# Kernel optimization log

Hardware: AMD Instinct MI355X
Metric: run time of the kernel (lower is better)

The kernel has to match this reference:

```python
import jax, jax.numpy as jnp
import numpy as np

# SOM hyperparameters (match init_kwargs)
M, N = 64, 64
NODES = M * N
FEATS = 256
BATCH = 1024
LR = 0.5
RADIUS_FACTOR = 1.1
TOTAL_ITER = 100000
SIGMA = max(M, N) * RADIUS_FACTOR


def setup_inputs() -> dict:
    key = jax.random.key(0)
    k1, k2 = jax.random.split(key)
    x = jax.random.uniform(k1, (BATCH, FEATS), dtype=jnp.float32)
    map_w = jax.random.uniform(k2, (NODES, FEATS), dtype=jnp.float32)
    return {"x": x, "map_w": map_w, "iteration": 0}


def _grid_locs():
    ii, jj = jnp.meshgrid(jnp.arange(M), jnp.arange(N), indexing='ij')
    return jnp.stack([ii.ravel(), jj.ravel()], axis=1)  # (NODES, 2) int32


def reference(x, map_w, iteration):
    B = x.shape[0]
    # ---- feedforward: squared distances (B, NODES) via GEMM expansion,
    # avoiding the (B, NODES, FEATS) broadcast the TF code materializes.
    x2 = jnp.sum(x * x, axis=1, keepdims=True)          # (B, 1)
    w2 = jnp.sum(map_w * map_w, axis=1)                  # (NODES,)
    sqd = x2 + w2[None, :] - 2.0 * (x @ map_w.T)         # (B, NODES)
    bmu_indices = jnp.argmin(sqd, axis=1)                # (B,)

    # ---- backprop: neighborhood-weighted codebook update
    locs = _grid_locs()                                  # (NODES, 2)
    bmu_locs = locs[bmu_indices]                         # (B, 2)
    # grid distance^2 between every node and each sample's BMU: (B, NODES)
    d2 = jnp.sum((locs[None, :, :] - bmu_locs[:, None, :]) ** 2, axis=2).astype(jnp.float32)

    lambda_g = TOTAL_ITER / SIGMA
    decay = jnp.exp(jnp.float32(-float(iteration) / lambda_g))
    radius = SIGMA * decay + 1e-6
    lr = LR * decay

    impact = jnp.exp(-d2 / (2.0 * radius * radius))
    in_radius = (jnp.sqrt(d2) <= radius).astype(jnp.float32)
    lr_op = impact * in_radius * lr                      # (B, NODES)

    # weight_update[n,d] = sum_b lr_op[b,n] * (x[b,d] - map_w[n,d])
    # computed without the (B, NODES, FEATS) intermediate:
    upd = (jnp.einsum('bn,bd->nd', lr_op, x) - lr_op.sum(axis=0)[:, None] * map_w) / B
    new_map = map_w + upd
    return new_map, bmu_indices
```

## Files before the change

kernel.cpp:

```cpp
#include <hip/hip_runtime.h>
#include <math.h>

#define NODES 4096
#define FEATS 256
#define BATCH 1024
#define LR_C 0.5f
#define SIGMA_C 70.4f

typedef _Float16 f16x8 __attribute__((ext_vector_type(8)));
typedef float floatx4 __attribute__((ext_vector_type(4)));

__device__ __forceinline__ void get_params(int it, float& lr, float& r2, float& i2r2) {
    float decay = __expf(-(float)it * (SIGMA_C / 100000.0f));
    float radius = SIGMA_C * decay + 1e-6f;
    lr = LR_C * decay;
    r2 = radius * radius;
    i2r2 = 1.0f / (2.0f * r2);
}

__device__ __forceinline__ unsigned fkey(float f) {
    unsigned u = __float_as_uint(f);
    return (u & 0x80000000u) ? ~u : (u | 0x80000000u);
}
__device__ __forceinline__ unsigned long long shfl_xor_u64(unsigned long long v, int mask) {
    unsigned lo = (unsigned)v, hi = (unsigned)(v >> 32);
    lo = __shfl_xor(lo, mask, 64);
    hi = __shfl_xor(hi, mask, 64);
    return ((unsigned long long)hi << 32) | lo;
}

__global__ __launch_bounds__(256) void k_prep(const float* __restrict__ Wm, const float* __restrict__ X,
                                              _Float16* __restrict__ Whi, _Float16* __restrict__ Wlo,
                                              float* __restrict__ w2,
                                              _Float16* __restrict__ Xhi, _Float16* __restrict__ Xlo,
                                              _Float16* __restrict__ XT,
                                              unsigned long long* __restrict__ gmin) {
    __shared__ _Float16 T[64][72];
    const int t = threadIdx.x;
    const int blk = blockIdx.x;
    const int wave = t >> 6, lane = t & 63;
#pragma unroll
    for (int rr = 0; rr < 2; ++rr) {
        int row = blk * 8 + wave * 2 + rr;
        float4 v = *(const float4*)&Wm[(size_t)row * FEATS + lane * 4];
        union { _Float16 h[4]; float2 f2; } uh, ul;
        uh.h[0] = (_Float16)v.x; uh.h[1] = (_Float16)v.y;
        uh.h[2] = (_Float16)v.z; uh.h[3] = (_Float16)v.w;
        ul.h[0] = (_Float16)(v.x - (float)uh.h[0]);
        ul.h[1] = (_Float16)(v.y - (float)uh.h[1]);
        ul.h[2] = (_Float16)(v.z - (float)uh.h[2]);
        ul.h[3] = (_Float16)(v.w - (float)uh.h[3]);
        *(float2*)&Whi[(size_t)row * FEATS + lane * 4] = uh.f2;
        *(float2*)&Wlo[(size_t)row * FEATS + lane * 4] = ul.f2;
        float s = v.x * v.x + v.y * v.y + v.z * v.z + v.w * v.w;
#pragma unroll
        for (int off = 32; off > 0; off >>= 1) s += __shfl_down(s, off, 64);
        if (lane == 0) w2[row] = s;
    }
    if (blk < 4) gmin[blk * 256 + t] = 0xFFFFFFFFFFFFFFFFULL;
    if (blk < 64) {
        const int b0 = (blk & 15) * 64, d0 = (blk >> 4) * 64;
        {
            const int bl = t >> 2, dq = (t & 3) * 16;
            union { _Float16 h[16]; float4 q[2]; } uh, ul;
#pragma unroll
            for (int c = 0; c < 4; ++c) {
                float4 v = *(const float4*)&X[(size_t)(b0 + bl) * FEATS + d0 + dq + c * 4];
                uh.h[c * 4 + 0] = (_Float16)v.x; uh.h[c * 4 + 1] = (_Float16)v.y;
                uh.h[c * 4 + 2] = (_Float16)v.z; uh.h[c * 4 + 3] = (_Float16)v.w;
                ul.h[c * 4 + 0] = (_Float16)(v.x - (float)uh.h[c * 4 + 0]);
                ul.h[c * 4 + 1] = (_Float16)(v.y - (float)uh.h[c * 4 + 1]);
                ul.h[c * 4 + 2] = (_Float16)(v.z - (float)uh.h[c * 4 + 2]);
                ul.h[c * 4 + 3] = (_Float16)(v.w - (float)uh.h[c * 4 + 3]);
            }
            *(float4*)&Xhi[(size_t)(b0 + bl) * FEATS + d0 + dq] = uh.q[0];
            *(float4*)&Xhi[(size_t)(b0 + bl) * FEATS + d0 + dq + 8] = uh.q[1];
            *(float4*)&Xlo[(size_t)(b0 + bl) * FEATS + d0 + dq] = ul.q[0];
            *(float4*)&Xlo[(size_t)(b0 + bl) * FEATS + d0 + dq + 8] = ul.q[1];
#pragma unroll
            for (int c = 0; c < 16; ++c) T[bl][dq + c] = uh.h[c];
        }
        __syncthreads();
        {
            const int dl = t >> 2, bq = (t & 3) * 16;
            union { _Float16 h[16]; float4 q[2]; } u;
#pragma unroll
            for (int c = 0; c < 16; ++c) u.h[c] = T[bq + c][dl];
            *(float4*)&XT[(size_t)(d0 + dl) * BATCH + b0 + bq] = u.q[0];
            *(float4*)&XT[(size_t)(d0 + dl) * BATCH + b0 + bq + 8] = u.q[1];
        }
    }
}

__global__ __launch_bounds__(256) void k_gemm1min(const _Float16* __restrict__ Xhi, const _Float16* __restrict__ Xlo,
                                                  const _Float16* __restrict__ Whi, const _Float16* __restrict__ Wlo,
                                                  const float* __restrict__ w2,
                                                  unsigned long long* __restrict__ gmin) {
    __shared__ _Float16 Ah[64][40];
    __shared__ _Float16 Al[64][40];
    __shared__ _Float16 Bh[64][40];
    __shared__ _Float16 Bl[64][40];
    __shared__ unsigned long long rowmin[64][2];
    const int n0 = blockIdx.x * 64;
    const int b0 = blockIdx.y * 64;
    const int t = threadIdx.x;
    const int wave = t >> 6, lane = t & 63;
    const int wm = wave & 1, wn = wave >> 1;
    const int lm = lane & 15, quad = lane >> 4;
    const int srow = t >> 2, skoff = (t & 3) * 8;
    floatx4 acc[2][2] = {};
    for (int k0 = 0; k0 < FEATS; k0 += 32) {
        *(float4*)&Ah[srow][skoff] = *(const float4*)&Xhi[(size_t)(b0 + srow) * FEATS + k0 + skoff];
        *(float4*)&Al[srow][skoff] = *(const float4*)&Xlo[(size_t)(b0 + srow) * FEATS + k0 + skoff];
        *(float4*)&Bh[srow][skoff] = *(const float4*)&Whi[(size_t)(n0 + srow) * FEATS + k0 + skoff];
        *(float4*)&Bl[srow][skoff] = *(const float4*)&Wlo[(size_t)(n0 + srow) * FEATS + k0 + skoff];
        __syncthreads();
        f16x8 ah[2], al[2], bh[2], bl[2];
        ah[0] = *(f16x8*)&Ah[wm * 32 + lm][quad * 8];
        ah[1] = *(f16x8*)&Ah[wm * 32 + 16 + lm][quad * 8];
        al[0] = *(f16x8*)&Al[wm * 32 + lm][quad * 8];
        al[1] = *(f16x8*)&Al[wm * 32 + 16 + lm][quad * 8];
        bh[0] = *(f16x8*)&Bh[wn * 32 + lm][quad * 8];
        bh[1] = *(f16x8*)&Bh[wn * 32 + 16 + lm][quad * 8];
        bl[0] = *(f16x8*)&Bl[wn * 32 + lm][quad * 8];
        bl[1] = *(f16x8*)&Bl[wn * 32 + 16 + lm][quad * 8];
#pragma unroll
        for (int i = 0; i < 2; ++i)
#pragma unroll
            for (int j = 0; j < 2; ++j) {
                acc[i][j] = __builtin_amdgcn_mfma_f32_16x16x32_f16(ah[i], bh[j], acc[i][j], 0, 0, 0);
                acc[i][j] = __builtin_amdgcn_mfma_f32_16x16x32_f16(ah[i], bl[j], acc[i][j], 0, 0, 0);
                acc[i][j] = __builtin_amdgcn_mfma_f32_16x16x32_f16(al[i], bh[j], acc[i][j], 0, 0, 0);
            }
        __syncthreads();
    }
    const int col0 = n0 + wn * 32 + lm, col1 = col0 + 16;
    const float w20 = w2[col0], w21 = w2[col1];
#pragma unroll
    for (int i = 0; i < 2; ++i) {
#pragma unroll
        for (int r = 0; r < 4; ++r) {
            float va = w20 - 2.0f * acc[i][0][r];
            float vb = w21 - 2.0f * acc[i][1][r];
            unsigned long long ka = ((unsigned long long)fkey(va) << 32) | (unsigned)col0;
            unsigned long long kb = ((unsigned long long)fkey(vb) << 32) | (unsigned)col1;
            unsigned long long m = ka < kb ? ka : kb;
#pragma unroll
            for (int mk = 1; mk < 16; mk <<= 1) {
                unsigned long long o = shfl_xor_u64(m, mk);
                if (o < m) m = o;
            }
            if (lm == 0) rowmin[wm * 32 + i * 16 + quad * 4 + r][wn] = m;
        }
    }
    __syncthreads();
    if (t < 64) {
        unsigned long long v = rowmin[t][0];
        if (rowmin[t][1] < v) v = rowmin[t][1];
        atomicMin(&gmin[b0 + t], v);
    }
}

__global__ __launch_bounds__(256) void k_lropB(const unsigned long long* __restrict__ gmin,
                                               const int* __restrict__ itp,
                                               _Float16* __restrict__ lrT, float* __restrict__ Svec,
                                               float* __restrict__ out1) {
    __shared__ int bmu_s[1024];
    __shared__ float texp[64];
    __shared__ float red4[4];
    const int t = threadIdx.x;
    const int blk = blockIdx.x;
#pragma unroll
    for (int j = 0; j < 4; ++j)
        bmu_s[t + j * 256] = (int)(gmin[t + j * 256] & 0xFFFFFFFFULL);
    float lr, r2, i2r2;
    get_params(itp[0], lr, r2, i2r2);
    if (t < 64) texp[t] = __expf(-(float)(t * t) * i2r2);
    __syncthreads();
    if (blk < 4) out1[blk * 256 + t] = (float)bmu_s[blk * 256 + t];
    const int n = blk * 2 + (t >> 7);
    const int b0 = (t & 127) * 8;
    const int ni = n >> 6, nj = n & 63;
    float s = 0.0f;
    union { _Float16 h[8]; float4 q; } u;
#pragma unroll
    for (int c = 0; c < 8; ++c) {
        int m = bmu_s[b0 + c];
        int di = ni - (m >> 6); di = di < 0 ? -di : di;
        int dj = nj - (m & 63); dj = dj < 0 ? -dj : dj;
        int d2 = di * di + dj * dj;
        float val = ((float)d2 <= r2) ? lr * texp[di] * texp[dj] : 0.0f;
        u.h[c] = (_Float16)val;
        s += val;
    }
    *(float4*)&lrT[(size_t)n * BATCH + b0] = u.q;
    const int lane = t & 63, wave = t >> 6;
#pragma unroll
    for (int off = 32; off > 0; off >>= 1) s += __shfl_down(s, off, 64);
    if (lane == 0) red4[wave] = s;
    __syncthreads();
    if (t < 2) Svec[blk * 2 + t] = red4[2 * t] + red4[2 * t + 1];
}

__global__ __launch_bounds__(256) void k_gemm2c(const _Float16* __restrict__ lrT, const _Float16* __restrict__ XT,
                                                const float* __restrict__ Svec, const float* __restrict__ Wm,
                                                float* __restrict__ out0) {
    __shared__ _Float16 As[32][136];
    __shared__ _Float16 Bs[64][136];
    __shared__ float Svl[32];
    const int d0 = blockIdx.x * 64;
    const int n0 = blockIdx.y * 32;
    const int t = threadIdx.x;
    const int wave = t >> 6, lane = t & 63;
    const int wm = wave & 1, wn = wave >> 1;
    const int lm = lane & 15, quad = lane >> 4;
    if (t < 32) Svl[t] = Svec[n0 + t];
    const int arow = t >> 3, acoff = (t & 7) * 16;
    const int brow = t >> 2, bcoff = (t & 3) * 32;
    floatx4 acc0 = {}, acc1 = {};
    for (int k0 = 0; k0 < BATCH; k0 += 128) {
        *(float4*)&As[arow][acoff] = *(const float4*)&lrT[(size_t)(n0 + arow) * BATCH + k0 + acoff];
        *(float4*)&As[arow][acoff + 8] = *(const float4*)&lrT[(size_t)(n0 + arow) * BATCH + k0 + acoff + 8];
#pragma unroll
        for (int c = 0; c < 4; ++c)
            *(float4*)&Bs[brow][bcoff + c * 8] =
                *(const float4*)&XT[(size_t)(d0 + brow) * BATCH + k0 + bcoff + c * 8];
        __syncthreads();
#pragma unroll
        for (int ks = 0; ks < 128; ks += 32) {
            f16x8 a = *(f16x8*)&As[wm * 16 + lm][ks + quad * 8];
            f16x8 b0 = *(f16x8*)&Bs[wn * 32 + lm][ks + quad * 8];
            f16x8 b1 = *(f16x8*)&Bs[wn * 32 + 16 + lm][ks + quad * 8];
            acc0 = __builtin_amdgcn_mfma_f32_16x16x32_f16(a, b0, acc0, 0, 0, 0);
            acc1 = __builtin_amdgcn_mfma_f32_16x16x32_f16(a, b1, acc1, 0, 0, 0);
        }
        __syncthreads();
    }
    const float invB = 1.0f / (float)BATCH;
#pragma unroll
    for (int r = 0; r < 4; ++r) {
        int rowN = n0 + wm * 16 + quad * 4 + r;
        float cc = 1.0f - Svl[rowN - n0] * invB;
        int col0 = d0 + wn * 32 + lm;
        int col1 = col0 + 16;
        out0[(size_t)rowN * FEATS + col0] = Wm[(size_t)rowN * FEATS + col0] * cc + acc0[r] * invB;
        out0[(size_t)rowN * FEATS + col1] = Wm[(size_t)rowN * FEATS + col1] * cc + acc1[r] * invB;
    }
}

extern "C" void kernel_launch(void* const* d_in, const int* in_sizes, int n_in,
                              void* d_out, int out_size, void* d_ws, size_t ws_size,
                              hipStream_t stream) {
    const float* X = (const float*)d_in[0];
    const float* Wm = (const float*)d_in[1];
    const int* itp = (const int*)d_in[2];
    float* out0 = (float*)d_out;
    float* out1 = out0 + (size_t)NODES * FEATS;

    char* ws = (char*)d_ws;
    float* w2       = (float*)(ws + 0);
    _Float16* Xhi   = (_Float16*)(ws + 16384);
    _Float16* Xlo   = (_Float16*)(ws + 540672);
    _Float16* XT    = (_Float16*)(ws + 1064960);
    _Float16* Whi   = (_Float16*)(ws + 1589248);
    _Float16* Wlo   = (_Float16*)(ws + 3686400);
    unsigned long long* gmin = (unsigned long long*)(ws + 5783552);
    float* Svec     = (float*)(ws + 5791744);
    _Float16* lrT   = (_Float16*)(ws + 5808128);

    k_prep<<<512, 256, 0, stream>>>(Wm, X, Whi, Wlo, w2, Xhi, Xlo, XT, gmin);
    k_gemm1min<<<dim3(64, 16), 256, 0, stream>>>(Xhi, Xlo, Whi, Wlo, w2, gmin);
    k_lropB<<<2048, 256, 0, stream>>>(gmin, itp, lrT, Svec, out1);
    k_gemm2c<<<dim3(4, 128), 256, 0, stream>>>(lrT, XT, Svec, Wm, out0);
}
```

Measured before the change: 95.84 us.

## Fuse fp16 split conversion into GEMM1 and merge XT transpose into lr kernel

Removes the separate prep kernel. GEMM1 now reads fp32 X and W directly, splits them into hi/lo fp16 in registers, and computes the W row norms on the fly. Its block tile grows to 128 rows with a per-wave atomicMin in place of the shared-memory row reduction. The X transpose to fp16 is appended as extra blocks of the lr-op kernel, and gmin is initialised with a memset. This saves one launch and the round trip of the fp16 copies through memory, at the cost of redoing the conversion in every GEMM block and issuing more atomics.

```diff
diff --git a/kernel.cpp b/kernel.cpp
--- a/kernel.cpp
+++ b/kernel.cpp
@@ -29,56 +29,158 @@
     return ((unsigned long long)hi << 32) | lo;
 }
 
-__global__ __launch_bounds__(256) void k_prep(const float* __restrict__ Wm, const float* __restrict__ X,
-                                              _Float16* __restrict__ Whi, _Float16* __restrict__ Wlo,
-                                              float* __restrict__ w2,
-                                              _Float16* __restrict__ Xhi, _Float16* __restrict__ Xlo,
-                                              _Float16* __restrict__ XT,
-                                              unsigned long long* __restrict__ gmin) {
-    __shared__ _Float16 T[64][72];
+__global__ __launch_bounds__(256) void k_gemm1min(const float* __restrict__ X, const float* __restrict__ Wm,
+                                                  unsigned long long* __restrict__ gmin) {
+    __shared__ _Float16 Ah[128][40];
+    __shared__ _Float16 Al[128][40];
+    __shared__ _Float16 Bh[64][40];
+    __shared__ _Float16 Bl[64][40];
+    __shared__ float w2s[64];
+    const int n0 = blockIdx.x * 64;
+    const int b0 = blockIdx.y * 128;
     const int t = threadIdx.x;
+    const int wave = t >> 6, lane = t & 63;
+    const int lm = lane & 15, quad = lane >> 4;
+    const int arow = t >> 1, ako = (t & 1) * 16;
+    const int brow = t >> 2, bko = (t & 3) * 8;
+    float w2p = 0.0f;
+    floatx4 acc[2][4] = {};
+    for (int k0 = 0; k0 < FEATS; k0 += 32) {
+        {
+            union { _Float16 h[16]; float4 q[2]; } uh, ul;
+#pragma unroll
+            for (int c = 0; c < 4; ++c) {
+                float4 v = *(const float4*)&X[(size_t)(b0 + arow) * FEATS + k0 + ako + c * 4];
+                _Float16 h0 = (_Float16)v.x, h1 = (_Float16)v.y, h2 = (_Float16)v.z, h3 = (_Float16)v.w;
+                uh.h[c * 4 + 0] = h0; uh.h[c * 4 + 1] = h1; uh.h[c * 4 + 2] = h2; uh.h[c * 4 + 3] = h3;
+                ul.h[c * 4 + 0] = (_Float16)(v.x - (float)h0);
+                ul.h[c * 4 + 1] = (_Float16)(v.y - (float)h1);
+                ul.h[c * 4 + 2] = (_Float16)(v.z - (float)h2);
+                ul.h[c * 4 + 3] = (_Float16)(v.w - (float)h3);
+            }
+            *(float4*)&Ah[arow][ako] = uh.q[0];
+            *(float4*)&Ah[arow][ako + 8] = uh.q[1];
+            *(float4*)&Al[arow][ako] = ul.q[0];
+            *(float4*)&Al[arow][ako + 8] = ul.q[1];
+        }
+        {
+            union { _Float16 h[8]; float4 q; } uh, ul;
+#pragma unroll
+            for (int c = 0; c < 2; ++c) {
+                float4 v = *(const float4*)&Wm[(size_t)(n0 + brow) * FEATS + k0 + bko + c * 4];
+                w2p += v.x * v.x + v.y * v.y + v.z * v.z + v.w * v.w;
+                _Float16 h0 = (_Float16)v.x, h1 = (_Float16)v.y, h2 = (_Float16)v.z, h3 = (_Float16)v.w;
+                uh.h[c * 4 + 0] = h0; uh.h[c * 4 + 1] = h1; uh.h[c * 4 + 2] = h2; uh.h[c * 4 + 3] = h3;
+                ul.h[c * 4 + 0] = (_Float16)(v.x - (float)h0);
+                ul.h[c * 4 + 1] = (_Float16)(v.y - (float)h1);
+                ul.h[c * 4 + 2] = (_Float16)(v.z - (float)h2);
+                ul.h[c * 4 + 3] = (_Float16)(v.w - (float)h3);
+            }
+            *(float4*)&Bh[brow][bko] = uh.q;
+            *(float4*)&Bl[brow][bko] = ul.q;
+        }
+        __syncthreads();
+        f16x8 ah[2], al[2], bh[4], bl[4];
+#pragma unroll
+        for (int i = 0; i < 2; ++i) {
+            ah[i] = *(f16x8*)&Ah[wave * 32 + i * 16 + lm][quad * 8];
+            al[i] = *(f16x8*)&Al[wave * 32 + i * 16 + lm][quad * 8];
+        }
+#pragma unroll
+        for (int j = 0; j < 4; ++j) {
+            bh[j] = *(f16x8*)&Bh[j * 16 + lm][quad * 8];
+            bl[j] = *(f16x8*)&Bl[j * 16 + lm][quad * 8];
+        }
+#pragma unroll
+        for (int i = 0; i < 2; ++i)
+#pragma unroll
+            for (int j = 0; j < 4; ++j) {
+                acc[i][j] = __builtin_amdgcn_mfma_f32_16x16x32_f16(ah[i], bh[j], acc[i][j], 0, 0, 0);
+                acc[i][j] = __builtin_amdgcn_mfma_f32_16x16x32_f16(ah[i], bl[j], acc[i][j], 0, 0, 0);
+                acc[i][j] = __builtin_amdgcn_mfma_f32_16x16x32_f16(al[i], bh[j], acc[i][j], 0, 0, 0);
+            }
+        __syncthreads();
+    }
+    w2p += __shfl_xor(w2p, 1, 64);
+    w2p += __shfl_xor(w2p, 2, 64);
+    if ((t & 3) == 0) w2s[brow] = w2p;
+    __syncthreads();
+#pragma unroll
+    for (int i = 0; i < 2; ++i)
+#pragma unroll
+        for (int r = 0; r < 4; ++r) {
+            const int row = b0 + wave * 32 + i * 16 + quad * 4 + r;
+            unsigned long long m = 0xFFFFFFFFFFFFFFFFULL;
+#pragma unroll
+            for (int j = 0; j < 4; ++j) {
+                float v = w2s[j * 16 + lm] - 2.0f * acc[i][j][r];
+                unsigned long long k = ((unsigned long long)fkey(v) << 32) | (unsigned)(n0 + j * 16 + lm);
+                if (k < m) m = k;
+            }
+#pragma unroll
+            for (int mk = 1; mk < 16; mk <<= 1) {
+                unsigned long long o = shfl_xor_u64(m, mk);
+                if (o < m) m = o;
+            }
+            if (lm == 0) atomicMin(&gmin[row], m);
+        }
+}
+
+__global__ __launch_bounds__(256) void k_lropX(const unsigned long long* __restrict__ gmin,
+                                               const int* __restrict__ itp, const float* __restrict__ X,
+                                               _Float16* __restrict__ lrT, float* __restrict__ Svec,
+                                               _Float16* __restrict__ XT, float* __restrict__ out1) {
     const int blk = blockIdx.x;
-    const int wave = t >> 6, lane = t & 63;
-#pragma unroll
-    for (int rr = 0; rr < 2; ++rr) {
-        int row = blk * 8 + wave * 2 + rr;
-        float4 v = *(const float4*)&Wm[(size_t)row * FEATS + lane * 4];
-        union { _Float16 h[4]; float2 f2; } uh, ul;
-        uh.h[0] = (_Float16)v.x; uh.h[1] = (_Float16)v.y;
-        uh.h[2] = (_Float16)v.z; uh.h[3] = (_Float16)v.w;
-        ul.h[0] = (_Float16)(v.x - (float)uh.h[0]);
-        ul.h[1] = (_Float16)(v.y - (float)uh.h[1]);
-        ul.h[2] = (_Float16)(v.z - (float)uh.h[2]);
-        ul.h[3] = (_Float16)(v.w - (float)uh.h[3]);
-        *(float2*)&Whi[(size_t)row * FEATS + lane * 4] = uh.f2;
-        *(float2*)&Wlo[(size_t)row * FEATS + lane * 4] = ul.f2;
-        float s = v.x * v.x + v.y * v.y + v.z * v.z + v.w * v.w;
+    const int t = threadIdx.x;
+    if (blk < 2048) {
+        __shared__ int bmu_s[1024];
+        __shared__ float texp[64];
+        __shared__ float red4[4];
+#pragma unroll
+        for (int j = 0; j < 4; ++j)
+            bmu_s[t + j * 256] = (int)(gmin[t + j * 256] & 0xFFFFFFFFULL);
+        float lr, r2, i2r2;
+        get_params(itp[0], lr, r2, i2r2);
+        if (t < 64) texp[t] = __expf(-(float)(t * t) * i2r2);
+        __syncthreads();
+        if (blk < 4) out1[blk * 256 + t] = (float)bmu_s[blk * 256 + t];
+        const int n = blk * 2 + (t >> 7);
+        const int b0 = (t & 127) * 8;
+        const int ni = n >> 6, nj = n & 63;
+        float s = 0.0f;
+        union { _Float16 h[8]; float4 q; } u;
+#pragma unroll
+        for (int c = 0; c < 8; ++c) {
+            int m = bmu_s[b0 + c];
+            int di = ni - (m >> 6); di = di < 0 ? -di : di;
+            int dj = nj - (m & 63); dj = dj < 0 ? -dj : dj;
+            int d2 = di * di + dj * dj;
+            float val = ((float)d2 <= r2) ? lr * texp[di] * texp[dj] : 0.0f;
+            u.h[c] = (_Float16)val;
+            s += val;
+        }
+        *(float4*)&lrT[(size_t)n * BATCH + b0] = u.q;
+        const int lane = t & 63, wave = t >> 6;
 #pragma unroll
         for (int off = 32; off > 0; off >>= 1) s += __shfl_down(s, off, 64);
-        if (lane == 0) w2[row] = s;
-    }
-    if (blk < 4) gmin[blk * 256 + t] = 0xFFFFFFFFFFFFFFFFULL;
-    if (blk < 64) {
-        const int b0 = (blk & 15) * 64, d0 = (blk >> 4) * 64;
+        if (lane == 0) red4[wave] = s;
+        __syncthreads();
+        if (t < 2) Svec[blk * 2 + t] = red4[2 * t] + red4[2 * t + 1];
+    } else {
+        __shared__ _Float16 T[64][72];
+        const int blk2 = blk - 2048;
+        const int b0 = (blk2 & 15) * 64, d0 = (blk2 >> 4) * 64;
         {
             const int bl = t >> 2, dq = (t & 3) * 16;
-            union { _Float16 h[16]; float4 q[2]; } uh, ul;
+            union { _Float16 h[16]; } u;
 #pragma unroll
             for (int c = 0; c < 4; ++c) {
                 float4 v = *(const float4*)&X[(size_t)(b0 + bl) * FEATS + d0 + dq + c * 4];
-                uh.h[c * 4 + 0] = (_Float16)v.x; uh.h[c * 4 + 1] = (_Float16)v.y;
-                uh.h[c * 4 + 2] = (_Float16)v.z; uh.h[c * 4 + 3] = (_Float16)v.w;
-                ul.h[c * 4 + 0] = (_Float16)(v.x - (float)uh.h[c * 4 + 0]);
-                ul.h[c * 4 + 1] = (_Float16)(v.y - (float)uh.h[c * 4 + 1]);
-                ul.h[c * 4 + 2] = (_Float16)(v.z - (float)uh.h[c * 4 + 2]);
-                ul.h[c * 4 + 3] = (_Float16)(v.w - (float)uh.h[c * 4 + 3]);
-            }
-            *(float4*)&Xhi[(size_t)(b0 + bl) * FEATS + d0 + dq] = uh.q[0];
-            *(float4*)&Xhi[(size_t)(b0 + bl) * FEATS + d0 + dq + 8] = uh.q[1];
-            *(float4*)&Xlo[(size_t)(b0 + bl) * FEATS + d0 + dq] = ul.q[0];
-            *(float4*)&Xlo[(size_t)(b0 + bl) * FEATS + d0 + dq + 8] = ul.q[1];
-#pragma unroll
-            for (int c = 0; c < 16; ++c) T[bl][dq + c] = uh.h[c];
+                u.h[c * 4 + 0] = (_Float16)v.x; u.h[c * 4 + 1] = (_Float16)v.y;
+                u.h[c * 4 + 2] = (_Float16)v.z; u.h[c * 4 + 3] = (_Float16)v.w;
+            }
+#pragma unroll
+            for (int c = 0; c < 16; ++c) T[bl][dq + c] = u.h[c];
         }
         __syncthreads();
         {
@@ -90,116 +192,6 @@
             *(float4*)&XT[(size_t)(d0 + dl) * BATCH + b0 + bq + 8] = u.q[1];
         }
     }
-}
-
-__global__ __launch_bounds__(256) void k_gemm1min(const _Float16* __restrict__ Xhi, const _Float16* __restrict__ Xlo,
-                                                  const _Float16* __restrict__ Whi, const _Float16* __restrict__ Wlo,
-                                                  const float* __restrict__ w2,
-                                                  unsigned long long* __restrict__ gmin) {
-    __shared__ _Float16 Ah[64][40];
-    __shared__ _Float16 Al[64][40];
-    __shared__ _Float16 Bh[64][40];
-    __shared__ _Float16 Bl[64][40];
-    __shared__ unsigned long long rowmin[64][2];
-    const int n0 = blockIdx.x * 64;
-    const int b0 = blockIdx.y * 64;
-    const int t = threadIdx.x;
-    const int wave = t >> 6, lane = t & 63;
-    const int wm = wave & 1, wn = wave >> 1;
-    const int lm = lane & 15, quad = lane >> 4;
-    const int srow = t >> 2, skoff = (t & 3) * 8;
-    floatx4 acc[2][2] = {};
-    for (int k0 = 0; k0 < FEATS; k0 += 32) {
-        *(float4*)&Ah[srow][skoff] = *(const float4*)&Xhi[(size_t)(b0 + srow) * FEATS + k0 + skoff];
-        *(float4*)&Al[srow][skoff] = *(const float4*)&Xlo[(size_t)(b0 + srow) * FEATS + k0 + skoff];
-        *(float4*)&Bh[srow][skoff] = *(const float4*)&Whi[(size_t)(n0 + srow) * FEATS + k0 + skoff];
-        *(float4*)&Bl[srow][skoff] = *(const float4*)&Wlo[(size_t)(n0 + srow) * FEATS + k0 + skoff];
-        __syncthreads();
-        f16x8 ah[2], al[2], bh[2], bl[2];
-        ah[0] = *(f16x8*)&Ah[wm * 32 + lm][quad * 8];
-        ah[1] = *(f16x8*)&Ah[wm * 32 + 16 + lm][quad * 8];
-        al[0] = *(f16x8*)&Al[wm * 32 + lm][quad * 8];
-        al[1] = *(f16x8*)&Al[wm * 32 + 16 + lm][quad * 8];
-        bh[0] = *(f16x8*)&Bh[wn * 32 + lm][quad * 8];
-        bh[1] = *(f16x8*)&Bh[wn * 32 + 16 + lm][quad * 8];
-        bl[0] = *(f16x8*)&Bl[wn * 32 + lm][quad * 8];
-        bl[1] = *(f16x8*)&Bl[wn * 32 + 16 + lm][quad * 8];
-#pragma unroll
-        for (int i = 0; i < 2; ++i)
-#pragma unroll
-            for (int j = 0; j < 2; ++j) {
-                acc[i][j] = __builtin_amdgcn_mfma_f32_16x16x32_f16(ah[i], bh[j], acc[i][j], 0, 0, 0);
-                acc[i][j] = __builtin_amdgcn_mfma_f32_16x16x32_f16(ah[i], bl[j], acc[i][j], 0, 0, 0);
-                acc[i][j] = __builtin_amdgcn_mfma_f32_16x16x32_f16(al[i], bh[j], acc[i][j], 0, 0, 0);
-            }
-        __syncthreads();
-    }
-    const int col0 = n0 + wn * 32 + lm, col1 = col0 + 16;
-    const float w20 = w2[col0], w21 = w2[col1];
-#pragma unroll
-    for (int i = 0; i < 2; ++i) {
-#pragma unroll
-        for (int r = 0; r < 4; ++r) {
-            float va = w20 - 2.0f * acc[i][0][r];
-            float vb = w21 - 2.0f * acc[i][1][r];
-            unsigned long long ka = ((unsigned long long)fkey(va) << 32) | (unsigned)col0;
-            unsigned long long kb = ((unsigned long long)fkey(vb) << 32) | (unsigned)col1;
-            unsigned long long m = ka < kb ? ka : kb;
-#pragma unroll
-            for (int mk = 1; mk < 16; mk <<= 1) {
-                unsigned long long o = shfl_xor_u64(m, mk);
-                if (o < m) m = o;
-            }
-            if (lm == 0) rowmin[wm * 32 + i * 16 + quad * 4 + r][wn] = m;
-        }
-    }
-    __syncthreads();
-    if (t < 64) {
-        unsigned long long v = rowmin[t][0];
-        if (rowmin[t][1] < v) v = rowmin[t][1];
-        atomicMin(&gmin[b0 + t], v);
-    }
-}
-
-__global__ __launch_bounds__(256) void k_lropB(const unsigned long long* __restrict__ gmin,
-                                               const int* __restrict__ itp,
-                                               _Float16* __restrict__ lrT, float* __restrict__ Svec,
-                                               float* __restrict__ out1) {
-    __shared__ int bmu_s[1024];
-    __shared__ float texp[64];
-    __shared__ float red4[4];
-    const int t = threadIdx.x;
-    const int blk = blockIdx.x;
-#pragma unroll
-    for (int j = 0; j < 4; ++j)
-        bmu_s[t + j * 256] = (int)(gmin[t + j * 256] & 0xFFFFFFFFULL);
-    float lr, r2, i2r2;
-    get_params(itp[0], lr, r2, i2r2);
-    if (t < 64) texp[t] = __expf(-(float)(t * t) * i2r2);
-    __syncthreads();
-    if (blk < 4) out1[blk * 256 + t] = (float)bmu_s[blk * 256 + t];
-    const int n = blk * 2 + (t >> 7);
-    const int b0 = (t & 127) * 8;
-    const int ni = n >> 6, nj = n & 63;
-    float s = 0.0f;
-    union { _Float16 h[8]; float4 q; } u;
-#pragma unroll
-    for (int c = 0; c < 8; ++c) {
-        int m = bmu_s[b0 + c];
-        int di = ni - (m >> 6); di = di < 0 ? -di : di;
-        int dj = nj - (m & 63); dj = dj < 0 ? -dj : dj;
-        int d2 = di * di + dj * dj;
-        float val = ((float)d2 <= r2) ? lr * texp[di] * texp[dj] : 0.0f;
-        u.h[c] = (_Float16)val;
-        s += val;
-    }
-    *(float4*)&lrT[(size_t)n * BATCH + b0] = u.q;
-    const int lane = t & 63, wave = t >> 6;
-#pragma unroll
-    for (int off = 32; off > 0; off >>= 1) s += __shfl_down(s, off, 64);
-    if (lane == 0) red4[wave] = s;
-    __syncthreads();
-    if (t < 2) Svec[blk * 2 + t] = red4[2 * t] + red4[2 * t + 1];
 }
 
 __global__ __launch_bounds__(256) void k_gemm2c(const _Float16* __restrict__ lrT, const _Float16* __restrict__ XT,
@@ -258,18 +250,13 @@
     float* out1 = out0 + (size_t)NODES * FEATS;
 
     char* ws = (char*)d_ws;
-    float* w2       = (float*)(ws + 0);
-    _Float16* Xhi   = (_Float16*)(ws + 16384);
-    _Float16* Xlo   = (_Float16*)(ws + 540672);
-    _Float16* XT    = (_Float16*)(ws + 1064960);
-    _Float16* Whi   = (_Float16*)(ws + 1589248);
-    _Float16* Wlo   = (_Float16*)(ws + 3686400);
-    unsigned long long* gmin = (unsigned long long*)(ws + 5783552);
-    float* Svec     = (float*)(ws + 5791744);
-    _Float16* lrT   = (_Float16*)(ws + 5808128);
-
-    k_prep<<<512, 256, 0, stream>>>(Wm, X, Whi, Wlo, w2, Xhi, Xlo, XT, gmin);
-    k_gemm1min<<<dim3(64, 16), 256, 0, stream>>>(Xhi, Xlo, Whi, Wlo, w2, gmin);
-    k_lropB<<<2048, 256, 0, stream>>>(gmin, itp, lrT, Svec, out1);
+    unsigned long long* gmin = (unsigned long long*)(ws + 0);
+    float* Svec     = (float*)(ws + 8192);
+    _Float16* XT    = (_Float16*)(ws + 24576);
+    _Float16* lrT   = (_Float16*)(ws + 548864);
+
+    hipMemsetAsync(gmin, 0xFF, 1024 * sizeof(unsigned long long), stream);
+    k_gemm1min<<<dim3(64, 8), 256, 0, stream>>>(X, Wm, gmin);
+    k_lropX<<<2112, 256, 0, stream>>>(gmin, itp, X, lrT, Svec, XT, out1);
     k_gemm2c<<<dim3(4, 128), 256, 0, stream>>>(lrT, XT, Svec, Wm, out0);
 }
```

Result: no change. 96.53 us (+0.7%).
